# Kernel tuning notes

Hardware: AMD Instinct MI355X
Metric: run time of the kernel (lower is better)

## Reference

```python
import jax, jax.numpy as jnp
import numpy as np
import math

C = 128          # sphere_channels
TIME_DIM = 64    # time_embed_dim
HID = 128        # time_mlp_hidden
B = 512          # num systems
N = 200000       # num atoms


def setup_inputs() -> dict:
    key = jax.random.key(0)
    ks = jax.random.split(key, 12)
    x = jax.random.normal(ks[0], (N, 9, C), dtype=jnp.float32)
    t = jax.random.uniform(ks[1], (B,), dtype=jnp.float32)
    batch_idx = jnp.sort(jax.random.randint(ks[2], (N,), 0, B))
    s = lambda k, shp: jax.random.normal(k, shp, dtype=jnp.float32) * 0.05
    # time MLP (note: module zero-inits the last layer; we randomize to exercise the math)
    tm_w1 = s(ks[3], (HID, TIME_DIM)); tm_b1 = s(ks[4], (HID,))
    tm_w2 = s(ks[5], (2 * C, HID));    tm_b2 = s(ks[6], (2 * C,))
    # SO3_Linear(C->C, lmax=1): per-degree weights, bias only on l=0
    lw = s(ks[7], (2, C, C)); lb = s(ks[8], (C,))
    # UMAGate gate projection
    gw = s(ks[9], (C, C)); gb = s(ks[10], (C,))
    # final SO3_Linear(C->1, lmax=1)
    fw = s(ks[11], (2, 1, C)); fb = jnp.zeros((1,), dtype=jnp.float32)
    return {"x": x, "t": t, "batch_idx": batch_idx,
            "tm_w1": tm_w1, "tm_b1": tm_b1, "tm_w2": tm_w2, "tm_b2": tm_b2,
            "lw": lw, "lb": lb, "gw": gw, "gb": gb, "fw": fw, "fb": fb}


def _time_embed(t):
    half = TIME_DIM // 2
    freqs = jnp.exp(-math.log(10000.0) * jnp.arange(half, dtype=t.dtype) / half)
    args = t[:, None] * freqs  # (B, half)
    return jnp.concatenate([jnp.sin(args), jnp.cos(args)], axis=-1)  # (B, TIME_DIM)


def _so3_linear(h, w, b):
    # h: (N, 4, Cin); w: (2, Cout, Cin); bias b only on l=0
    o0 = jnp.einsum('nc,oc->no', h[:, 0, :], w[0]) + b      # (N, Cout)
    o1 = jnp.einsum('nlc,oc->nlo', h[:, 1:4, :], w[1])      # (N, 3, Cout)
    return jnp.concatenate([o0[:, None, :], o1], axis=1)    # (N, 4, Cout)


def reference(x, t, batch_idx, tm_w1, tm_b1, tm_w2, tm_b2, lw, lb, gw, gb, fw, fb):
    # slice l=0..1 components: indices 0..3 of the (lmax+1)^2 axis
    x_l01 = x[:, 0:4, :]  # (N, 4, C)
    # time MLP -> per-system FiLM params
    t_emb = _time_embed(t)                                     # (B, TIME_DIM)
    hmid = jax.nn.silu(t_emb @ tm_w1.T + tm_b1)                # (B, HID)
    t_params = hmid @ tm_w2.T + tm_b2                          # (B, 2C)
    t_bias, t_scale = t_params[:, :C], t_params[:, C:]
    t_gate = 1.0 + t_scale
    # gather per-atom conditioning
    bias_pa = t_bias[batch_idx]                                # (N, C)
    gate_pa = t_gate[batch_idx]                                # (N, C)
    h_l0 = x_l01[:, 0, :] + bias_pa                            # (N, C)
    h_l1 = x_l01[:, 1:4, :] * gate_pa[:, None, :]              # (N, 3, C)
    h = jnp.concatenate([h_l0[:, None, :], h_l1], axis=1)      # (N, 4, C)
    # depth-1 = 1 hidden block: SO3_Linear + UMAGate
    h = _so3_linear(h, lw, lb)
    g = jax.nn.sigmoid(h[:, 0, :] @ gw.T + gb)                 # (N, C)
    h = jnp.concatenate([jax.nn.silu(h[:, 0, :])[:, None, :],
                         h[:, 1:4, :] * g[:, None, :]], axis=1)
    # final SO3_Linear(C -> 1)
    out = _so3_linear(h, fw, fb)                               # (N, 4, 1)
    return out[:, 1:4, :].reshape(-1, 3)                       # (N, 3)
```

## Files before the change

### kernel.cpp

```cpp
#include <hip/hip_runtime.h>
#include <cstdint>
#include <cstddef>


#define TPT 64

__global__ __launch_bounds__(256) void k_prep(const float* __restrict__ lw,
                                              const float* __restrict__ lb,
                                              const float* __restrict__ gw,
                                              const float* __restrict__ gb,
                                              float* __restrict__ ws) {
  int gid = blockIdx.x;
  if (gid < 64) {
    int g = gid * 256 + threadIdx.x;
    int c = g & 127, o = g >> 7;
    const float* lw0 = lw;
    float acc = 0.f;
    #pragma unroll 4
    for (int j = 0; j < 128; ++j) acc += gw[o * 128 + j] * lw0[j * 128 + c];
    ws[c * 128 + o] = acc;
  } else {
    int o = threadIdx.x;
    if (o < 128) {
      float acc = gb[o];
      for (int j = 0; j < 128; ++j) acc += gw[o * 128 + j] * lb[j];
      ws[16384 + o] = acc;
    }
  }
}

__global__ __launch_bounds__(128) void k_time(const float* __restrict__ t,
                                              const float* __restrict__ w1,
                                              const float* __restrict__ b1,
                                              const float* __restrict__ w2,
                                              const float* __restrict__ b2,
                                              float* __restrict__ ws, int B) {
  __shared__ float temb[64];
  __shared__ float hm[128];
  __shared__ float tb[128];
  int b = blockIdx.x;
  int h = threadIdx.x;
  float tv = t[b];
  if (h < 32) {
    float fr = expf(-9.210340371976184f * (float)h / 32.f);
    float arg = tv * fr;
    temb[h] = sinf(arg);
    temb[32 + h] = cosf(arg);
  }
  __syncthreads();
  float pre = b1[h];
  #pragma unroll 4
  for (int d = 0; d < 64; ++d) pre += temb[d] * w1[h * 64 + d];
  hm[h] = pre / (1.f + expf(-pre));
  __syncthreads();
  float p0 = b2[h], p1 = b2[128 + h];
  #pragma unroll 4
  for (int d = 0; d < 128; ++d) {
    float hv = hm[d];
    p0 += hv * w2[h * 128 + d];
    p1 += hv * w2[(128 + h) * 128 + d];
  }
  tb[h] = p0;
  float* gate_g = ws + 16512;
  float* bb_g   = gate_g + (size_t)B * 128;
  gate_g[b * 128 + h] = 1.f + p1;
  __syncthreads();
  float acc = ws[16384 + h];
  #pragma unroll 4
  for (int c = 0; c < 128; ++c) acc += ws[c * 128 + h] * tb[c];
  bb_g[b * 128 + h] = acc;
}

__global__ __launch_bounds__(512, 2) void k_main(const float* __restrict__ x,
                                                 const int* __restrict__ bidx,
                                                 const float* __restrict__ lw,
                                                 const float* __restrict__ fw,
                                                 const float* __restrict__ ws,
                                                 float* __restrict__ out,
                                                 int N, int NTiles, int B) {
  __shared__ __align__(16) float W1[128 * 128];
  __shared__ __align__(16) float W2[128 * 128];
  __shared__ __align__(16) float XB[64 * 128];

  const int tid = threadIdx.x;
  const int tx = tid & 31;
  const int ty = tid >> 5;

  {
    const float4* s1 = (const float4*)ws;
    const float4* s2 = (const float4*)(lw + 16384);
    float4* d1 = (float4*)W1;
    float4* d2 = (float4*)W2;
    #pragma unroll
    for (int i = 0; i < 8; ++i) {
      d1[tid + i * 512] = s1[tid + i * 512];
      d2[tid + i * 512] = s2[tid + i * 512];
    }
  }
  const float* gate_g = ws + 16512;
  const float* bb_g   = gate_g + (size_t)B * 128;

  float4 f1r = *(const float4*)(fw + 128 + 4 * tx);

  float4 st[4];
  const int grid = (int)gridDim.x;

  auto issue_stage = [&](int tt) {
    int n0 = tt * TPT;
    #pragma unroll
    for (int i = 0; i < 4; ++i) {
      int idx = tid + i * 512;
      int p = idx >> 5, c4 = idx & 31;
      int n = n0 + p; if (n >= N) n = N - 1;
      st[i] = *(const float4*)(x + (size_t)n * 1152 + c4 * 4);
    }
  };
  auto write_stage = [&]() {
    float4* xb4 = (float4*)XB;
    #pragma unroll
    for (int i = 0; i < 4; ++i) xb4[tid + i * 512] = st[i];
  };

  int t0 = blockIdx.x;
  if (t0 < NTiles) { issue_stage(t0); write_stage(); }

  for (int t = t0; t < NTiles; t += grid) {
    __syncthreads();
    const int n0 = t * TPT;

    int bi[4];
    float acc[4][4];
    #pragma unroll
    for (int pj = 0; pj < 4; ++pj) {
      int n = n0 + 4 * ty + pj; if (n >= N) n = N - 1;
      bi[pj] = bidx[n];
      float4 br = *(const float4*)(bb_g + (size_t)bi[pj] * 128 + 4 * tx);
      acc[0][pj] = br.x; acc[1][pj] = br.y; acc[2][pj] = br.z; acc[3][pj] = br.w;
    }

    {
      const float4* w1p = (const float4*)W1;
      const float* xb0 = XB + (4 * ty) * 128;
      #pragma unroll 4
      for (int k4 = 0; k4 < 32; ++k4) {
        float ar[4][4];
        #pragma unroll
        for (int pj = 0; pj < 4; ++pj)
          *(float4*)&ar[pj][0] = *(const float4*)(xb0 + pj * 128 + k4 * 4);
        #pragma unroll
        for (int u = 0; u < 4; ++u) {
          float4 w = w1p[(k4 * 4 + u) * 32 + tx];
          #pragma unroll
          for (int pj = 0; pj < 4; ++pj) {
            float xv = ar[pj][u];
            acc[0][pj] += w.x * xv; acc[1][pj] += w.y * xv;
            acc[2][pj] += w.z * xv; acc[3][pj] += w.w * xv;
          }
        }
      }
    }

    float wv[4][4];
    #pragma unroll
    for (int oj = 0; oj < 4; ++oj) {
      float fo = (oj == 0) ? f1r.x : (oj == 1) ? f1r.y : (oj == 2) ? f1r.z : f1r.w;
      #pragma unroll
      for (int pj = 0; pj < 4; ++pj) {
        float g = 1.f / (1.f + __expf(-acc[oj][pj]));
        wv[oj][pj] = g * fo;
      }
    }

    __syncthreads();
    #pragma unroll
    for (int pj = 0; pj < 4; ++pj) {
      int p = 4 * ty + pj;
      float4 q = make_float4(wv[0][pj], wv[1][pj], wv[2][pj], wv[3][pj]);
      ((float4*)XB)[p * 32 + (tx ^ (p & 7))] = q;
    }
    __syncthreads();

    float ac2[4][4];
    #pragma unroll
    for (int cj = 0; cj < 4; ++cj)
      #pragma unroll
      for (int pj = 0; pj < 4; ++pj) ac2[cj][pj] = 0.f;
    {
      const float4* w2p = (const float4*)W2;
      const float4* wx4 = (const float4*)XB;
      #pragma unroll 4
      for (int o4 = 0; o4 < 32; ++o4) {
        float a2r[4][4];
        #pragma unroll
        for (int pj = 0; pj < 4; ++pj) {
          int p = 4 * ty + pj;
          *(float4*)&a2r[pj][0] = *(const float4*)&wx4[p * 32 + (o4 ^ (p & 7))];
        }
        #pragma unroll
        for (int u = 0; u < 4; ++u) {
          float4 w = w2p[(o4 * 4 + u) * 32 + tx];
          #pragma unroll
          for (int pj = 0; pj < 4; ++pj) {
            float wvv = a2r[pj][u];
            ac2[0][pj] += w.x * wvv; ac2[1][pj] += w.y * wvv;
            ac2[2][pj] += w.z * wvv; ac2[3][pj] += w.w * wvv;
          }
        }
      }
    }
    __syncthreads();

    bool more = (t + grid) < NTiles;
    if (more) issue_stage(t + grid);

    #pragma unroll
    for (int pj = 0; pj < 4; ++pj) {
      float4 gr = *(const float4*)(gate_g + (size_t)bi[pj] * 128 + 4 * tx);
      ac2[0][pj] *= gr.x; ac2[1][pj] *= gr.y; ac2[2][pj] *= gr.z; ac2[3][pj] *= gr.w;
    }

    float part[4][3];
    #pragma unroll
    for (int pj = 0; pj < 4; ++pj) {
      int n = n0 + 4 * ty + pj;
      int nc = n >= N ? N - 1 : n;
      #pragma unroll
      for (int l = 0; l < 3; ++l) {
        float4 xr = *(const float4*)(x + (size_t)nc * 1152 + (1 + l) * 128 + 4 * tx);
        part[pj][l] = xr.x * ac2[0][pj] + xr.y * ac2[1][pj] +
                      xr.z * ac2[2][pj] + xr.w * ac2[3][pj];
      }
    }
    #pragma unroll
    for (int m = 1; m < 32; m <<= 1)
      #pragma unroll
      for (int pj = 0; pj < 4; ++pj)
        #pragma unroll
        for (int l = 0; l < 3; ++l)
          part[pj][l] += __shfl_xor(part[pj][l], m, 64);

    if (tx == 0) {
      if (n0 + TPT <= N) {
        float4* ob = (float4*)(out + (size_t)(n0 + 4 * ty) * 3);
        ob[0] = make_float4(part[0][0], part[0][1], part[0][2], part[1][0]);
        ob[1] = make_float4(part[1][1], part[1][2], part[2][0], part[2][1]);
        ob[2] = make_float4(part[2][2], part[3][0], part[3][1], part[3][2]);
      } else {
        #pragma unroll
        for (int pj = 0; pj < 4; ++pj) {
          int n = n0 + 4 * ty + pj;
          if (n < N) {
            out[(size_t)n * 3 + 0] = part[pj][0];
            out[(size_t)n * 3 + 1] = part[pj][1];
            out[(size_t)n * 3 + 2] = part[pj][2];
          }
        }
      }
    }

    if (more) write_stage();
  }
}

extern "C" void kernel_launch(void* const* d_in, const int* in_sizes, int n_in,
                              void* d_out, int out_size, void* d_ws, size_t ws_size,
                              hipStream_t stream) {
  const float* x      = (const float*)d_in[0];
  const float* t      = (const float*)d_in[1];
  const int*   bidx   = (const int*)d_in[2];
  const float* tm_w1  = (const float*)d_in[3];
  const float* tm_b1  = (const float*)d_in[4];
  const float* tm_w2  = (const float*)d_in[5];
  const float* tm_b2  = (const float*)d_in[6];
  const float* lw     = (const float*)d_in[7];
  const float* lb     = (const float*)d_in[8];
  const float* gw     = (const float*)d_in[9];
  const float* gb     = (const float*)d_in[10];
  const float* fw     = (const float*)d_in[11];

  float* out = (float*)d_out;
  float* ws  = (float*)d_ws;

  int N = in_sizes[0] / (9 * 128);
  int B = in_sizes[1];
  int NTiles = (N + TPT - 1) / TPT;

  hipLaunchKernelGGL(k_prep, dim3(65), dim3(256), 0, stream, lw, lb, gw, gb, ws);
  hipLaunchKernelGGL(k_time, dim3(B), dim3(128), 0, stream,
                     t, tm_w1, tm_b1, tm_w2, tm_b2, ws, B);
  int grid = NTiles < 256 ? NTiles : 256;
  hipLaunchKernelGGL(k_main, dim3(grid), dim3(512), 0, stream,
                     x, bidx, lw, fw, ws, out, N, NTiles, B);
}
```

Baseline: 1.352 ms.

## Stream weights via scalar loads, async LDS staging, contiguous tile ranges

Restructures k_main so each wave owns 16 output channels and each lane one atom. The 128x128 weight matrices are no longer copied into shared memory; their wave-uniform addresses allow scalar (SMEM) loads. x tiles go straight from global memory into LDS with global_load_lds using a swizzled layout, and the cross-lane shuffle reduction is replaced by an LDS partial-sum reduction across the 8 waves. The smaller LDS footprint allows 4 blocks per CU and a grid of 512 with contiguous tile ranges per block. The risk is higher register pressure under the 4-block launch bound and more scalar-cache traffic for the weights.

```diff
diff --git a/kernel.cpp b/kernel.cpp
--- a/kernel.cpp
+++ b/kernel.cpp
@@ -71,194 +71,151 @@
   bb_g[b * 128 + h] = acc;
 }
 
-__global__ __launch_bounds__(512, 2) void k_main(const float* __restrict__ x,
+__device__ __forceinline__ void gload_lds16(const void* g, void* l) {
+  __builtin_amdgcn_global_load_lds(
+      (const __attribute__((address_space(1))) void*)g,
+      (__attribute__((address_space(3))) void*)l, 16, 0, 0);
+}
+
+__global__ __launch_bounds__(512, 4) void k_main(const float* __restrict__ x,
                                                  const int* __restrict__ bidx,
                                                  const float* __restrict__ lw,
                                                  const float* __restrict__ fw,
                                                  const float* __restrict__ ws,
                                                  float* __restrict__ out,
                                                  int N, int NTiles, int B) {
-  __shared__ __align__(16) float W1[128 * 128];
-  __shared__ __align__(16) float W2[128 * 128];
-  __shared__ __align__(16) float XB[64 * 128];
+  __shared__ __align__(16) float XB[TPT * 128];
+  __shared__ __align__(16) float WX[TPT * 128];
+  __shared__ float PS[8 * TPT * 3];
 
   const int tid = threadIdx.x;
-  const int tx = tid & 31;
-  const int ty = tid >> 5;
-
-  {
-    const float4* s1 = (const float4*)ws;
-    const float4* s2 = (const float4*)(lw + 16384);
-    float4* d1 = (float4*)W1;
-    float4* d2 = (float4*)W2;
-    #pragma unroll
-    for (int i = 0; i < 8; ++i) {
-      d1[tid + i * 512] = s1[tid + i * 512];
-      d2[tid + i * 512] = s2[tid + i * 512];
-    }
-  }
+  const int wv_ = tid >> 6;
+  const int p   = tid & 63;
+  const int ps  = p & 7;
+  const int ob  = __builtin_amdgcn_readfirstlane(wv_ * 16);
+
+  const float* __restrict__ w1w = ws + ob;
+  const float* __restrict__ w2w = lw + 16384 + ob;
   const float* gate_g = ws + 16512;
   const float* bb_g   = gate_g + (size_t)B * 128;
 
-  float4 f1r = *(const float4*)(fw + 128 + 4 * tx);
-
-  float4 st[4];
-  const int grid = (int)gridDim.x;
-
-  auto issue_stage = [&](int tt) {
+  float f1[16];
+  #pragma unroll
+  for (int i = 0; i < 4; ++i)
+    *(float4*)&f1[4 * i] = *(const float4*)(fw + 128 + ob + 4 * i);
+
+  auto stage = [&](int tt) {
     int n0 = tt * TPT;
     #pragma unroll
     for (int i = 0; i < 4; ++i) {
-      int idx = tid + i * 512;
-      int p = idx >> 5, c4 = idx & 31;
-      int n = n0 + p; if (n >= N) n = N - 1;
-      st[i] = *(const float4*)(x + (size_t)n * 1152 + c4 * 4);
+      int S  = (wv_ * 4 + i) * 64 + p;
+      int sp = S >> 5, sj = S & 31;
+      int n = n0 + sp; if (n >= N) n = N - 1;
+      const float* src = x + (size_t)n * 1152 + ((sj ^ (sp & 7)) << 2);
+      gload_lds16(src, XB + (size_t)(wv_ * 4 + i) * 256);
     }
   };
-  auto write_stage = [&]() {
-    float4* xb4 = (float4*)XB;
-    #pragma unroll
-    for (int i = 0; i < 4; ++i) xb4[tid + i * 512] = st[i];
-  };
-
-  int t0 = blockIdx.x;
-  if (t0 < NTiles) { issue_stage(t0); write_stage(); }
-
-  for (int t = t0; t < NTiles; t += grid) {
+
+  int nb   = (int)gridDim.x;
+  int bpc  = NTiles / nb, rem = NTiles % nb;
+  int bsel = (int)blockIdx.x;
+  int tstart = bsel * bpc + (bsel < rem ? bsel : rem);
+  int tcnt   = bpc + (bsel < rem ? 1 : 0);
+  int tend   = tstart + tcnt;
+  if (tcnt <= 0) return;
+
+  stage(tstart);
+
+  for (int t = tstart; t < tend; ++t) {
+    const int n0 = t * TPT;
+    asm volatile("s_waitcnt vmcnt(0)" ::: "memory");
     __syncthreads();
-    const int n0 = t * TPT;
-
-    int bi[4];
-    float acc[4][4];
-    #pragma unroll
-    for (int pj = 0; pj < 4; ++pj) {
-      int n = n0 + 4 * ty + pj; if (n >= N) n = N - 1;
-      bi[pj] = bidx[n];
-      float4 br = *(const float4*)(bb_g + (size_t)bi[pj] * 128 + 4 * tx);
-      acc[0][pj] = br.x; acc[1][pj] = br.y; acc[2][pj] = br.z; acc[3][pj] = br.w;
-    }
-
-    {
-      const float4* w1p = (const float4*)W1;
-      const float* xb0 = XB + (4 * ty) * 128;
-      #pragma unroll 4
-      for (int k4 = 0; k4 < 32; ++k4) {
-        float ar[4][4];
-        #pragma unroll
-        for (int pj = 0; pj < 4; ++pj)
-          *(float4*)&ar[pj][0] = *(const float4*)(xb0 + pj * 128 + k4 * 4);
-        #pragma unroll
-        for (int u = 0; u < 4; ++u) {
-          float4 w = w1p[(k4 * 4 + u) * 32 + tx];
-          #pragma unroll
-          for (int pj = 0; pj < 4; ++pj) {
-            float xv = ar[pj][u];
-            acc[0][pj] += w.x * xv; acc[1][pj] += w.y * xv;
-            acc[2][pj] += w.z * xv; acc[3][pj] += w.w * xv;
-          }
-        }
+
+    int n = n0 + p; if (n >= N) n = N - 1;
+    const int bi = bidx[n];
+
+    float acc[16];
+    #pragma unroll
+    for (int i = 0; i < 4; ++i) {
+      float4 b4 = *(const float4*)(bb_g + (size_t)bi * 128 + ob + 4 * i);
+      acc[4 * i + 0] = b4.x; acc[4 * i + 1] = b4.y;
+      acc[4 * i + 2] = b4.z; acc[4 * i + 3] = b4.w;
+    }
+    #pragma unroll 4
+    for (int k4 = 0; k4 < 32; ++k4) {
+      float4 xv = *(const float4*)(XB + p * 128 + ((k4 ^ ps) << 2));
+      const float* wr = w1w + (size_t)(k4 * 4) * 128;
+      #pragma unroll
+      for (int j = 0; j < 16; ++j) acc[j] = fmaf(wr[j], xv.x, acc[j]);
+      #pragma unroll
+      for (int j = 0; j < 16; ++j) acc[j] = fmaf(wr[128 + j], xv.y, acc[j]);
+      #pragma unroll
+      for (int j = 0; j < 16; ++j) acc[j] = fmaf(wr[256 + j], xv.z, acc[j]);
+      #pragma unroll
+      for (int j = 0; j < 16; ++j) acc[j] = fmaf(wr[384 + j], xv.w, acc[j]);
+    }
+
+    #pragma unroll
+    for (int i = 0; i < 4; ++i) {
+      float4 q;
+      q.x = f1[4 * i + 0] / (1.f + __expf(-acc[4 * i + 0]));
+      q.y = f1[4 * i + 1] / (1.f + __expf(-acc[4 * i + 1]));
+      q.z = f1[4 * i + 2] / (1.f + __expf(-acc[4 * i + 2]));
+      q.w = f1[4 * i + 3] / (1.f + __expf(-acc[4 * i + 3]));
+      *(float4*)(WX + p * 128 + (((wv_ * 4 + i) ^ ps) << 2)) = q;
+    }
+    __syncthreads();
+
+    if (t + 1 < tend) stage(t + 1);
+
+    float ac2[16];
+    #pragma unroll
+    for (int j = 0; j < 16; ++j) ac2[j] = 0.f;
+    #pragma unroll 4
+    for (int o4 = 0; o4 < 32; ++o4) {
+      float4 wxv = *(const float4*)(WX + p * 128 + ((o4 ^ ps) << 2));
+      const float* wr = w2w + (size_t)(o4 * 4) * 128;
+      #pragma unroll
+      for (int j = 0; j < 16; ++j) ac2[j] = fmaf(wr[j], wxv.x, ac2[j]);
+      #pragma unroll
+      for (int j = 0; j < 16; ++j) ac2[j] = fmaf(wr[128 + j], wxv.y, ac2[j]);
+      #pragma unroll
+      for (int j = 0; j < 16; ++j) ac2[j] = fmaf(wr[256 + j], wxv.z, ac2[j]);
+      #pragma unroll
+      for (int j = 0; j < 16; ++j) ac2[j] = fmaf(wr[384 + j], wxv.w, ac2[j]);
+    }
+
+    #pragma unroll
+    for (int i = 0; i < 4; ++i) {
+      float4 g4 = *(const float4*)(gate_g + (size_t)bi * 128 + ob + 4 * i);
+      ac2[4 * i + 0] *= g4.x; ac2[4 * i + 1] *= g4.y;
+      ac2[4 * i + 2] *= g4.z; ac2[4 * i + 3] *= g4.w;
+    }
+    float part[3];
+    const float* xb1 = x + (size_t)n * 1152 + 128 + ob;
+    #pragma unroll
+    for (int l = 0; l < 3; ++l) {
+      float s = 0.f;
+      #pragma unroll
+      for (int i = 0; i < 4; ++i) {
+        float4 x4 = *(const float4*)(xb1 + l * 128 + 4 * i);
+        s += x4.x * ac2[4 * i + 0] + x4.y * ac2[4 * i + 1] +
+             x4.z * ac2[4 * i + 2] + x4.w * ac2[4 * i + 3];
       }
-    }
-
-    float wv[4][4];
-    #pragma unroll
-    for (int oj = 0; oj < 4; ++oj) {
-      float fo = (oj == 0) ? f1r.x : (oj == 1) ? f1r.y : (oj == 2) ? f1r.z : f1r.w;
-      #pragma unroll
-      for (int pj = 0; pj < 4; ++pj) {
-        float g = 1.f / (1.f + __expf(-acc[oj][pj]));
-        wv[oj][pj] = g * fo;
-      }
-    }
-
+      part[l] = s;
+    }
+    PS[(wv_ * 64 + p) * 3 + 0] = part[0];
+    PS[(wv_ * 64 + p) * 3 + 1] = part[1];
+    PS[(wv_ * 64 + p) * 3 + 2] = part[2];
     __syncthreads();
-    #pragma unroll
-    for (int pj = 0; pj < 4; ++pj) {
-      int p = 4 * ty + pj;
-      float4 q = make_float4(wv[0][pj], wv[1][pj], wv[2][pj], wv[3][pj]);
-      ((float4*)XB)[p * 32 + (tx ^ (p & 7))] = q;
-    }
-    __syncthreads();
-
-    float ac2[4][4];
-    #pragma unroll
-    for (int cj = 0; cj < 4; ++cj)
-      #pragma unroll
-      for (int pj = 0; pj < 4; ++pj) ac2[cj][pj] = 0.f;
-    {
-      const float4* w2p = (const float4*)W2;
-      const float4* wx4 = (const float4*)XB;
-      #pragma unroll 4
-      for (int o4 = 0; o4 < 32; ++o4) {
-        float a2r[4][4];
-        #pragma unroll
-        for (int pj = 0; pj < 4; ++pj) {
-          int p = 4 * ty + pj;
-          *(float4*)&a2r[pj][0] = *(const float4*)&wx4[p * 32 + (o4 ^ (p & 7))];
-        }
-        #pragma unroll
-        for (int u = 0; u < 4; ++u) {
-          float4 w = w2p[(o4 * 4 + u) * 32 + tx];
-          #pragma unroll
-          for (int pj = 0; pj < 4; ++pj) {
-            float wvv = a2r[pj][u];
-            ac2[0][pj] += w.x * wvv; ac2[1][pj] += w.y * wvv;
-            ac2[2][pj] += w.z * wvv; ac2[3][pj] += w.w * wvv;
-          }
-        }
-      }
-    }
-    __syncthreads();
-
-    bool more = (t + grid) < NTiles;
-    if (more) issue_stage(t + grid);
-
-    #pragma unroll
-    for (int pj = 0; pj < 4; ++pj) {
-      float4 gr = *(const float4*)(gate_g + (size_t)bi[pj] * 128 + 4 * tx);
-      ac2[0][pj] *= gr.x; ac2[1][pj] *= gr.y; ac2[2][pj] *= gr.z; ac2[3][pj] *= gr.w;
-    }
-
-    float part[4][3];
-    #pragma unroll
-    for (int pj = 0; pj < 4; ++pj) {
-      int n = n0 + 4 * ty + pj;
-      int nc = n >= N ? N - 1 : n;
-      #pragma unroll
-      for (int l = 0; l < 3; ++l) {
-        float4 xr = *(const float4*)(x + (size_t)nc * 1152 + (1 + l) * 128 + 4 * tx);
-        part[pj][l] = xr.x * ac2[0][pj] + xr.y * ac2[1][pj] +
-                      xr.z * ac2[2][pj] + xr.w * ac2[3][pj];
-      }
-    }
-    #pragma unroll
-    for (int m = 1; m < 32; m <<= 1)
-      #pragma unroll
-      for (int pj = 0; pj < 4; ++pj)
-        #pragma unroll
-        for (int l = 0; l < 3; ++l)
-          part[pj][l] += __shfl_xor(part[pj][l], m, 64);
-
-    if (tx == 0) {
-      if (n0 + TPT <= N) {
-        float4* ob = (float4*)(out + (size_t)(n0 + 4 * ty) * 3);
-        ob[0] = make_float4(part[0][0], part[0][1], part[0][2], part[1][0]);
-        ob[1] = make_float4(part[1][1], part[1][2], part[2][0], part[2][1]);
-        ob[2] = make_float4(part[2][2], part[3][0], part[3][1], part[3][2]);
-      } else {
-        #pragma unroll
-        for (int pj = 0; pj < 4; ++pj) {
-          int n = n0 + 4 * ty + pj;
-          if (n < N) {
-            out[(size_t)n * 3 + 0] = part[pj][0];
-            out[(size_t)n * 3 + 1] = part[pj][1];
-            out[(size_t)n * 3 + 2] = part[pj][2];
-          }
-        }
-      }
-    }
-
-    if (more) write_stage();
+
+    if (tid < 192) {
+      int q = tid / 3, l = tid - q * 3;
+      float s = 0.f;
+      #pragma unroll
+      for (int w2 = 0; w2 < 8; ++w2) s += PS[(w2 * 64 + q) * 3 + l];
+      if (n0 + q < N) out[(size_t)n0 * 3 + tid] = s;
+    }
   }
 }
 
@@ -288,7 +245,7 @@
   hipLaunchKernelGGL(k_prep, dim3(65), dim3(256), 0, stream, lw, lb, gw, gb, ws);
   hipLaunchKernelGGL(k_time, dim3(B), dim3(128), 0, stream,
                      t, tm_w1, tm_b1, tm_w2, tm_b2, ws, B);
-  int grid = NTiles < 256 ? NTiles : 256;
+  int grid = NTiles < 512 ? NTiles : 512;
   hipLaunchKernelGGL(k_main, dim3(grid), dim3(512), 0, stream,
                      x, bidx, lw, fw, ws, out, N, NTiles, B);
 }
```

Measured after the change: 1.244 ms. 8.0% less time.
